# Optimization experiments

Measured on AMD Instinct MI355X. Metric: run time of the kernel, lower is better.

The kernel has to match this reference:

```python
import jax, jax.numpy as jnp
import numpy as np

B, S, D, H = 4, 2048, 1024, 16
HD = D // H


def setup_inputs() -> dict:
    key = jax.random.key(0)
    ks = jax.random.split(key, 5)
    scale = 1.0 / np.sqrt(D)
    return {
        "x": jax.random.normal(ks[0], (B, S, D), dtype=jnp.float32),
        "W_q": jax.random.normal(ks[1], (D, D), dtype=jnp.float32) * scale,
        "W_k": jax.random.normal(ks[2], (D, D), dtype=jnp.float32) * scale,
        "W_v": jax.random.normal(ks[3], (D, D), dtype=jnp.float32) * scale,
        "W_o": jax.random.normal(ks[4], (D, D), dtype=jnp.float32) * scale,
    }


def reference(x, W_q, W_k, W_v, W_o):
    # Linear with weight [out, in]: y = x @ W^T
    def proj(W):
        return jnp.einsum('bsd,ed->bshf', x, W.reshape(H, HD, D).transpose(0, 1, 2).reshape(D, D)) if False else (x @ W.T).reshape(B, S, H, HD).transpose(0, 2, 1, 3)

    q = proj(W_q)  # [B, H, S, HD]
    k = proj(W_k)
    v = proj(W_v)

    scores = jnp.einsum('bhqd,bhkd->bhqk', q, k) / jnp.sqrt(jnp.float32(HD))
    causal = jnp.triu(jnp.ones((S, S), dtype=bool), k=1)  # True above diagonal -> masked
    scores = jnp.where(causal, -jnp.inf, scores)
    probs = jax.nn.softmax(scores, axis=-1)
    out = jnp.einsum('bhqk,bhkd->bhqd', probs, v)  # [B, H, S, HD]
    out = out.transpose(0, 2, 1, 3).reshape(B, S, D)
    return out @ W_o.T
```

## Files before the change

### kernel.cpp

```cpp
#include <hip/hip_runtime.h>
#include <cstdint>
#include <cstddef>

typedef unsigned short u16;
typedef __attribute__((ext_vector_type(8))) short short8;
typedef __attribute__((ext_vector_type(4))) short short4v;
typedef __attribute__((ext_vector_type(8))) unsigned short ushort8v;
typedef __attribute__((ext_vector_type(4))) unsigned short ushort4v;
typedef __attribute__((ext_vector_type(4))) unsigned int uint4v;
typedef __attribute__((ext_vector_type(4))) float f32x4;

#define QSCALE 0.18033688011112042f
#define THR_L2 11.5417f


__device__ __forceinline__ u16 f2bf(float f) {
  unsigned int u = __builtin_bit_cast(unsigned int, f);
  u += 0x7FFFu + ((u >> 16) & 1u);
  return (u16)(u >> 16);
}

__device__ __forceinline__ void async16(const void* g, void* l) {
  __builtin_amdgcn_global_load_lds(
      (const __attribute__((address_space(1))) unsigned int*)g,
      (__attribute__((address_space(3))) unsigned int*)l, 16, 0, 0);
}

__device__ __forceinline__ float fmax3(float a, float b, float c) {
  float r;
  asm("v_max3_f32 %0, %1, %2, %3" : "=v"(r) : "v"(a), "v"(b), "v"(c));
  return r;
}

__device__ __forceinline__ unsigned int cvtpk(float lo, float hi) {
  unsigned int r;
  asm("v_cvt_pk_bf16_f32 %0, %1, %2" : "=v"(r) : "v"(lo), "v"(hi));
  return r;
}


__global__ void cvt_all(const float* __restrict__ x, const float* __restrict__ Wq,
                        const float* __restrict__ Wk, const float* __restrict__ Wv,
                        const float* __restrict__ Wo, u16* __restrict__ out) {
  const int bid = blockIdx.x;
  const float* src;
  int i;
  size_t doff;
  if (bid < 8192) {
    i = bid * 1024 + threadIdx.x * 4;
    src = x;
    doff = (size_t)i;
  } else {
    const int k = bid - 8192;
    const int wsel = k >> 10;
    i = (k & 1023) * 1024 + threadIdx.x * 4;
    src = (wsel == 0) ? Wq : (wsel == 1) ? Wk : (wsel == 2) ? Wv : Wo;
    doff = 8388608 + (size_t)wsel * 1048576 + i;
  }
  float4 v = *(const float4*)(src + i);
  ushort4v o;
  o[0] = f2bf(v.x); o[1] = f2bf(v.y); o[2] = f2bf(v.z); o[3] = f2bf(v.w);
  *(ushort4v*)(out + doff) = o;
}


template<int MODE>
__global__ __launch_bounds__(256, 3) void gemm_bt(
    const u16* __restrict__ A, const u16* __restrict__ Bw,
    void* __restrict__ Cout, int M, int N, int K)
{
  const int t = threadIdx.x;
  const int lane = t & 63, w = t >> 6;
  const int li = lane & 15, g = lane >> 4;
  const int wr = w >> 1, wc = w & 1;

  const int nx = gridDim.x;
  const int hwid = blockIdx.y * nx + blockIdx.x;
  const int cpx = (nx * gridDim.y) >> 3;
  const int lid = (hwid & 7) * cpx + (hwid >> 3);
  const int brow = (lid / nx) * 128, bcol = (lid % nx) * 128;

  __shared__ u16 As[128 * 32];
  __shared__ u16 Bs[128 * 32];

  f32x4 acc[4][4];
#pragma unroll
  for (int i = 0; i < 4; ++i)
#pragma unroll
    for (int j = 0; j < 4; ++j) acc[i][j] = f32x4{0.f, 0.f, 0.f, 0.f};

  for (int k0 = 0; k0 < K; k0 += 32) {
#pragma unroll
    for (int L = 0; L < 2; ++L) {
      const int f = t + 256 * L;
      const int row = f >> 2;
      const int cb = ((f & 3) * 16) ^ ((row & 3) << 4);
      async16(A + (size_t)(brow + row) * K + k0 + (cb >> 1),
              &As[(w * 64 + 256 * L) * 8]);
      async16(Bw + (size_t)(bcol + row) * K + k0 + (cb >> 1),
              &Bs[(w * 64 + 256 * L) * 8]);
    }
    __syncthreads();
    short8 af[4], bfr[4];
    const int ksw = (g * 8) ^ ((li & 3) << 3);
#pragma unroll
    for (int mt = 0; mt < 4; ++mt)
      af[mt] = *(const short8*)&As[(wr * 64 + mt * 16 + li) * 32 + ksw];
#pragma unroll
    for (int nt = 0; nt < 4; ++nt)
      bfr[nt] = *(const short8*)&Bs[(wc * 64 + nt * 16 + li) * 32 + ksw];
    __builtin_amdgcn_s_setprio(1);
#pragma unroll
    for (int mt = 0; mt < 4; ++mt)
#pragma unroll
      for (int nt = 0; nt < 4; ++nt)
        acc[mt][nt] = __builtin_amdgcn_mfma_f32_16x16x32_bf16(af[mt], bfr[nt], acc[mt][nt], 0, 0, 0);
    __builtin_amdgcn_s_setprio(0);
    __syncthreads();
  }

#pragma unroll
  for (int mt = 0; mt < 4; ++mt)
#pragma unroll
    for (int nt = 0; nt < 4; ++nt) {
      const int col = bcol + wc * 64 + nt * 16 + li;
#pragma unroll
      for (int r = 0; r < 4; ++r) {
        const int row = brow + wr * 64 + mt * 16 + g * 4 + r;
        float v = acc[mt][nt][r];
        if (MODE == 0) {
          const int which = col >> 10;
          const int c2 = col & 1023;
          if (which == 0) v *= QSCALE;
          const int b = row >> 11, s = row & 2047;
          const int h = c2 >> 6, hd = c2 & 63;
          ((u16*)Cout)[(size_t)which * 8388608 +
                       (((size_t)(b * 16 + h) * 2048) + s) * 64 + hd] = f2bf(v);
        } else {
          ((float*)Cout)[(size_t)row * N + col] = v;
        }
      }
    }
}


__global__ __launch_bounds__(256) void transpose_hd_s(
    const u16* __restrict__ V, u16* __restrict__ VT)
{
  const int sb = blockIdx.x;
  const int bh = blockIdx.y;
  __shared__ u16 tile[64 * 72];
  const int t = threadIdx.x;
  const int r = t >> 3;
  const int c8 = (t & 7) * 8;
  const size_t base = (size_t)bh * 2048 * 64;
#pragma unroll
  for (int half = 0; half < 2; ++half) {
    const int row = r + 32 * half;
    ushort8v v = *(const ushort8v*)(V + base + (size_t)(sb * 64 + row) * 64 + c8);
    *(ushort8v*)&tile[row * 72 + c8] = v;
  }
  __syncthreads();
#pragma unroll
  for (int half = 0; half < 2; ++half) {
    const int hd = r + 32 * half;
    ushort8v o;
#pragma unroll
    for (int j = 0; j < 8; ++j) o[j] = tile[(c8 + j) * 72 + hd];
    *(ushort8v*)(VT + base + (size_t)hd * 2048 + sb * 64 + c8) = o;
  }
}


__global__ __launch_bounds__(256, 5) void flash_attn5(
    const u16* __restrict__ Qp, const u16* __restrict__ Kp,
    const u16* __restrict__ VTp, u16* __restrict__ Oattn)
{
  const int n = blockIdx.x;
  const int xcd = n & 7, sq = n >> 3;
  const int bh = xcd * 8 + (sq >> 4);
  const int pr = sq & 15;
  const int tile0 = pr, tile1 = 31 - pr;
  const int njb0 = pr + 1;

  const int t = threadIdx.x;
  const int lane = t & 63, w = t >> 6;
  const int li = lane & 15, g = lane >> 4;

  __shared__ u16 Kl[2][4096];
  __shared__ u16 Vl[2][4096];

  const size_t bh_off = (size_t)bh * (2048 * 64);
  const int b = bh >> 4, h = bh & 15;
  const int ksw = (li & 7) << 3;

  int qbase = tile0 * 64;

  f32x4 o_acc[4];
#pragma unroll
  for (int i = 0; i < 4; ++i) o_acc[i] = f32x4{0.f, 0.f, 0.f, 0.f};
  float m_i = -1e30f, l_i = 0.f;

  auto STAGE = [&](int i, int sb) {
    const int jb = (i < njb0) ? i : (i - njb0);
#pragma unroll
    for (int L = 0; L < 2; ++L) {
      const int f = t + 256 * L;
      const int kbyte = (f * 16) ^ (((f >> 3) & 7) << 4);
      async16(Kp + bh_off + (size_t)jb * 4096 + (kbyte >> 1),
              &Kl[sb][(w * 64 + 256 * L) * 8]);
      const int vrow = f >> 3;
      const int vb = ((f & 7) * 16) ^ ((vrow & 7) << 4);
      async16(VTp + bh_off + (size_t)vrow * 2048 + jb * 64 + (vb >> 1),
              &Vl[sb][(w * 64 + 256 * L) * 8]);
    }
  };

  auto WRITEO = [&]() {
    const float inv_l = 1.f / l_i;
    const int qrow = qbase + w * 16 + li;
    u16* op = Oattn + ((size_t)(b * 2048 + qrow)) * 1024 + h * 64;
#pragma unroll
    for (int dt = 0; dt < 4; ++dt) {
      ushort4v st;
#pragma unroll
      for (int r = 0; r < 4; ++r) st[r] = f2bf(o_acc[dt][r] * inv_l);
      *(ushort4v*)(op + dt * 16 + g * 4) = st;
    }
  };

  short8 qc[2];
  {
    const u16* qp = Qp + bh_off + (size_t)(qbase + w * 16 + li) * 64 + g * 8;
    qc[0] = *(const short8*)qp;
    qc[1] = *(const short8*)(qp + 32);
  }

  STAGE(0, 0);
  asm volatile("s_waitcnt vmcnt(0)" ::: "memory");
  __builtin_amdgcn_s_barrier();

#pragma unroll 1
  for (int i = 0; i < 33; ++i) {
    const int sb = i & 1;
    if (i + 1 < 33) STAGE(i + 1, (i + 1) & 1);

    const int jb = (i < njb0) ? i : (i - njb0);
    const u16* __restrict__ Ks = &Kl[sb][0];
    const u16* __restrict__ Vs = &Vl[sb][0];

    f32x4 s_acc[4];
#pragma unroll
    for (int jt = 0; jt < 4; ++jt) s_acc[jt] = f32x4{0.f, 0.f, 0.f, 0.f};
    __builtin_amdgcn_s_setprio(1);
#pragma unroll
    for (int kc = 0; kc < 2; ++kc)
#pragma unroll
      for (int jt = 0; jt < 4; ++jt) {
        short8 kf = *(const short8*)&Ks[(jt * 16 + li) * 64 + ((kc * 32 + g * 8) ^ ksw)];
        s_acc[jt] = __builtin_amdgcn_mfma_f32_16x16x32_bf16(kf, qc[kc], s_acc[jt], 0, 0, 0);
      }
    __builtin_amdgcn_s_setprio(0);

    if (jb * 64 + 63 > qbase + w * 16) {
      const int tq = qbase + w * 16 + li - jb * 64;
#pragma unroll
      for (int jt = 0; jt < 4; ++jt)
#pragma unroll
        for (int r = 0; r < 4; ++r)
          if (jt * 16 + g * 4 + r > tq) s_acc[jt][r] = -1e30f;
    }
    float t0 = fmax3(s_acc[0][0], s_acc[0][1], s_acc[0][2]);
    float t1 = fmax3(s_acc[0][3], s_acc[1][0], s_acc[1][1]);
    float t2 = fmax3(s_acc[1][2], s_acc[1][3], s_acc[2][0]);
    float t3 = fmax3(s_acc[2][1], s_acc[2][2], s_acc[2][3]);
    float t4m = fmax3(s_acc[3][0], s_acc[3][1], s_acc[3][2]);
    float m01 = fmax3(t0, t1, s_acc[3][3]);
    float m23 = fmax3(t2, t3, t4m);
    float mm = fmaxf(m01, m23);
    mm = fmaxf(mm, __shfl_xor(mm, 16));
    mm = fmaxf(mm, __shfl_xor(mm, 32));

    if (__any((int)(mm > m_i + THR_L2))) {
      const float mn = fmaxf(m_i, mm);
      const float corr = __builtin_amdgcn_exp2f(m_i - mn);
      l_i *= corr;
#pragma unroll
      for (int dt = 0; dt < 4; ++dt) o_acc[dt] *= corr;
      m_i = mn;
    }

    float ps = 0.f;
#pragma unroll
    for (int jt = 0; jt < 4; ++jt)
#pragma unroll
      for (int r = 0; r < 4; ++r) {
        float e = __builtin_amdgcn_exp2f(s_acc[jt][r] - m_i);
        s_acc[jt][r] = e;
        ps += e;
      }
    ps += __shfl_xor(ps, 16);
    ps += __shfl_xor(ps, 32);
    l_i += ps;
    short8 pf[2];
#pragma unroll
    for (int kc = 0; kc < 2; ++kc) {
      uint4v u;
      u[0] = cvtpk(s_acc[2 * kc][0], s_acc[2 * kc][1]);
      u[1] = cvtpk(s_acc[2 * kc][2], s_acc[2 * kc][3]);
      u[2] = cvtpk(s_acc[2 * kc + 1][0], s_acc[2 * kc + 1][1]);
      u[3] = cvtpk(s_acc[2 * kc + 1][2], s_acc[2 * kc + 1][3]);
      pf[kc] = __builtin_bit_cast(short8, u);
    }

    __builtin_amdgcn_s_setprio(1);
#pragma unroll
    for (int kc = 0; kc < 2; ++kc)
#pragma unroll
      for (int dt = 0; dt < 4; ++dt) {
        const int rowb = (dt * 16 + li) * 64;
        short4v v0 = *(const short4v*)&Vs[rowb + ((kc * 32 + g * 4) ^ ksw)];
        short4v v1 = *(const short4v*)&Vs[rowb + ((kc * 32 + 16 + g * 4) ^ ksw)];
        short8 vf = __builtin_shufflevector(v0, v1, 0, 1, 2, 3, 4, 5, 6, 7);
        o_acc[dt] = __builtin_amdgcn_mfma_f32_16x16x32_bf16(vf, pf[kc], o_acc[dt], 0, 0, 0);
      }
    __builtin_amdgcn_s_setprio(0);

    asm volatile("s_waitcnt lgkmcnt(0)" ::: "memory");
    asm volatile("s_waitcnt vmcnt(0)" ::: "memory");
    __builtin_amdgcn_s_barrier();

    if (i == njb0 - 1) {
      WRITEO();
      qbase = tile1 * 64;
      const u16* qp = Qp + bh_off + (size_t)(qbase + w * 16 + li) * 64 + g * 8;
      qc[0] = *(const short8*)qp;
      qc[1] = *(const short8*)(qp + 32);
      m_i = -1e30f; l_i = 0.f;
#pragma unroll
      for (int dt = 0; dt < 4; ++dt) o_acc[dt] = f32x4{0.f, 0.f, 0.f, 0.f};
    }
  }

  WRITEO();
}


extern "C" void kernel_launch(void* const* d_in, const int* in_sizes, int n_in,
                              void* d_out, int out_size, void* d_ws, size_t ws_size,
                              hipStream_t stream) {
  const float* x  = (const float*)d_in[0];
  const float* Wq = (const float*)d_in[1];
  const float* Wk = (const float*)d_in[2];
  const float* Wv = (const float*)d_in[3];
  const float* Wo = (const float*)d_in[4];

  const size_t NX = 8388608;
  const size_t NW = 1048576;

  u16* xb  = (u16*)d_ws;
  u16* wqb = xb + NX;
  u16* wob = wqb + 3 * NW;
  u16* Qb  = wob + NW;
  u16* Kb  = Qb + NX;
  u16* Vb  = Kb + NX;
  u16* VTb = Vb + NX;
  u16* attnb = Vb;

  cvt_all<<<12288, 256, 0, stream>>>(x, Wq, Wk, Wv, Wo, xb);

  gemm_bt<0><<<dim3(24, 64), 256, 0, stream>>>(xb, wqb, Qb, 8192, 3072, 1024);

  transpose_hd_s<<<dim3(32, 64), 256, 0, stream>>>(Vb, VTb);
  flash_attn5<<<1024, 256, 0, stream>>>(Qb, Kb, VTb, attnb);

  gemm_bt<1><<<dim3(8, 64), 256, 0, stream>>>(attnb, wob, d_out, 8192, 1024, 1024);
}
```

Before: 182.7 us.

## Rewrite flash attention with 128-row query tiles and direct global K/V loads

```diff
diff --git a/kernel.cpp b/kernel.cpp
--- a/kernel.cpp
+++ b/kernel.cpp
@@ -4,10 +4,10 @@
 
 typedef unsigned short u16;
 typedef __attribute__((ext_vector_type(8))) short short8;
-typedef __attribute__((ext_vector_type(4))) short short4v;
 typedef __attribute__((ext_vector_type(8))) unsigned short ushort8v;
 typedef __attribute__((ext_vector_type(4))) unsigned short ushort4v;
 typedef __attribute__((ext_vector_type(4))) unsigned int uint4v;
+typedef __attribute__((ext_vector_type(2))) unsigned int uint2v;
 typedef __attribute__((ext_vector_type(4))) float f32x4;
 
 #define QSCALE 0.18033688011112042f
@@ -172,173 +172,180 @@
 }
 
 
-__global__ __launch_bounds__(256, 5) void flash_attn5(
+__global__ __launch_bounds__(256, 2) void flash_attn8(
     const u16* __restrict__ Qp, const u16* __restrict__ Kp,
     const u16* __restrict__ VTp, u16* __restrict__ Oattn)
 {
-  const int n = blockIdx.x;
-  const int xcd = n & 7, sq = n >> 3;
-  const int bh = xcd * 8 + (sq >> 4);
-  const int pr = sq & 15;
-  const int tile0 = pr, tile1 = 31 - pr;
-  const int njb0 = pr + 1;
+  const int id = blockIdx.x;
+  const int x8 = id & 7, r8 = id >> 3;
+  const int bh = x8 * 8 + (r8 & 7);
+  const int p  = r8 >> 3;
+  const int tile1 = 15 - p;
+  const int njb0 = 2 * p + 2;
 
   const int t = threadIdx.x;
   const int lane = t & 63, w = t >> 6;
   const int li = lane & 15, g = lane >> 4;
 
-  __shared__ u16 Kl[2][4096];
-  __shared__ u16 Vl[2][4096];
-
   const size_t bh_off = (size_t)bh * (2048 * 64);
   const int b = bh >> 4, h = bh & 15;
-  const int ksw = (li & 7) << 3;
-
-  int qbase = tile0 * 64;
-
-  f32x4 o_acc[4];
-#pragma unroll
-  for (int i = 0; i < 4; ++i) o_acc[i] = f32x4{0.f, 0.f, 0.f, 0.f};
-  float m_i = -1e30f, l_i = 0.f;
-
-  auto STAGE = [&](int i, int sb) {
+
+  int q0 = p * 128 + w * 32;
+
+  short8 qf[2][2];
+  auto LOADQ = [&]() {
+#pragma unroll
+    for (int qn = 0; qn < 2; ++qn)
+#pragma unroll
+      for (int kc = 0; kc < 2; ++kc)
+        qf[qn][kc] = *(const short8*)(Qp + bh_off +
+            (size_t)(q0 + qn * 16 + li) * 64 + kc * 32 + g * 8);
+  };
+  LOADQ();
+
+  f32x4 o_acc[4][2];
+#pragma unroll
+  for (int dt = 0; dt < 4; ++dt)
+#pragma unroll
+    for (int qn = 0; qn < 2; ++qn) o_acc[dt][qn] = f32x4{0.f, 0.f, 0.f, 0.f};
+  float m_i[2] = {-1e30f, -1e30f};
+  float l_i[2] = {0.f, 0.f};
+
+  auto WRITEO = [&]() {
+#pragma unroll
+    for (int qn = 0; qn < 2; ++qn) {
+      const float inv = 1.f / l_i[qn];
+      u16* op = Oattn + ((size_t)(b * 2048 + q0 + qn * 16 + li)) * 1024 + h * 64;
+#pragma unroll
+      for (int dt = 0; dt < 4; ++dt) {
+        ushort4v st;
+#pragma unroll
+        for (int r = 0; r < 4; ++r) st[r] = f2bf(o_acc[dt][qn][r] * inv);
+        *(ushort4v*)(op + dt * 16 + g * 4) = st;
+      }
+    }
+  };
+
+#pragma unroll 1
+  for (int i = 0; i < 34; ++i) {
     const int jb = (i < njb0) ? i : (i - njb0);
-#pragma unroll
-    for (int L = 0; L < 2; ++L) {
-      const int f = t + 256 * L;
-      const int kbyte = (f * 16) ^ (((f >> 3) & 7) << 4);
-      async16(Kp + bh_off + (size_t)jb * 4096 + (kbyte >> 1),
-              &Kl[sb][(w * 64 + 256 * L) * 8]);
-      const int vrow = f >> 3;
-      const int vb = ((f & 7) * 16) ^ ((vrow & 7) << 4);
-      async16(VTp + bh_off + (size_t)vrow * 2048 + jb * 64 + (vb >> 1),
-              &Vl[sb][(w * 64 + 256 * L) * 8]);
-    }
-  };
-
-  auto WRITEO = [&]() {
-    const float inv_l = 1.f / l_i;
-    const int qrow = qbase + w * 16 + li;
-    u16* op = Oattn + ((size_t)(b * 2048 + qrow)) * 1024 + h * 64;
-#pragma unroll
-    for (int dt = 0; dt < 4; ++dt) {
-      ushort4v st;
-#pragma unroll
-      for (int r = 0; r < 4; ++r) st[r] = f2bf(o_acc[dt][r] * inv_l);
-      *(ushort4v*)(op + dt * 16 + g * 4) = st;
-    }
-  };
-
-  short8 qc[2];
-  {
-    const u16* qp = Qp + bh_off + (size_t)(qbase + w * 16 + li) * 64 + g * 8;
-    qc[0] = *(const short8*)qp;
-    qc[1] = *(const short8*)(qp + 32);
-  }
-
-  STAGE(0, 0);
-  asm volatile("s_waitcnt vmcnt(0)" ::: "memory");
-  __builtin_amdgcn_s_barrier();
-
-#pragma unroll 1
-  for (int i = 0; i < 33; ++i) {
-    const int sb = i & 1;
-    if (i + 1 < 33) STAGE(i + 1, (i + 1) & 1);
-
-    const int jb = (i < njb0) ? i : (i - njb0);
-    const u16* __restrict__ Ks = &Kl[sb][0];
-    const u16* __restrict__ Vs = &Vl[sb][0];
-
-    f32x4 s_acc[4];
-#pragma unroll
-    for (int jt = 0; jt < 4; ++jt) s_acc[jt] = f32x4{0.f, 0.f, 0.f, 0.f};
-    __builtin_amdgcn_s_setprio(1);
-#pragma unroll
-    for (int kc = 0; kc < 2; ++kc)
-#pragma unroll
-      for (int jt = 0; jt < 4; ++jt) {
-        short8 kf = *(const short8*)&Ks[(jt * 16 + li) * 64 + ((kc * 32 + g * 8) ^ ksw)];
-        s_acc[jt] = __builtin_amdgcn_mfma_f32_16x16x32_bf16(kf, qc[kc], s_acc[jt], 0, 0, 0);
-      }
-    __builtin_amdgcn_s_setprio(0);
-
-    if (jb * 64 + 63 > qbase + w * 16) {
-      const int tq = qbase + w * 16 + li - jb * 64;
-#pragma unroll
-      for (int jt = 0; jt < 4; ++jt)
-#pragma unroll
-        for (int r = 0; r < 4; ++r)
-          if (jt * 16 + g * 4 + r > tq) s_acc[jt][r] = -1e30f;
-    }
-    float t0 = fmax3(s_acc[0][0], s_acc[0][1], s_acc[0][2]);
-    float t1 = fmax3(s_acc[0][3], s_acc[1][0], s_acc[1][1]);
-    float t2 = fmax3(s_acc[1][2], s_acc[1][3], s_acc[2][0]);
-    float t3 = fmax3(s_acc[2][1], s_acc[2][2], s_acc[2][3]);
-    float t4m = fmax3(s_acc[3][0], s_acc[3][1], s_acc[3][2]);
-    float m01 = fmax3(t0, t1, s_acc[3][3]);
-    float m23 = fmax3(t2, t3, t4m);
-    float mm = fmaxf(m01, m23);
-    mm = fmaxf(mm, __shfl_xor(mm, 16));
-    mm = fmaxf(mm, __shfl_xor(mm, 32));
-
-    if (__any((int)(mm > m_i + THR_L2))) {
-      const float mn = fmaxf(m_i, mm);
-      const float corr = __builtin_amdgcn_exp2f(m_i - mn);
-      l_i *= corr;
-#pragma unroll
-      for (int dt = 0; dt < 4; ++dt) o_acc[dt] *= corr;
-      m_i = mn;
-    }
-
-    float ps = 0.f;
-#pragma unroll
-    for (int jt = 0; jt < 4; ++jt)
-#pragma unroll
-      for (int r = 0; r < 4; ++r) {
-        float e = __builtin_amdgcn_exp2f(s_acc[jt][r] - m_i);
-        s_acc[jt][r] = e;
-        ps += e;
-      }
-    ps += __shfl_xor(ps, 16);
-    ps += __shfl_xor(ps, 32);
-    l_i += ps;
-    short8 pf[2];
-#pragma unroll
-    for (int kc = 0; kc < 2; ++kc) {
-      uint4v u;
-      u[0] = cvtpk(s_acc[2 * kc][0], s_acc[2 * kc][1]);
-      u[1] = cvtpk(s_acc[2 * kc][2], s_acc[2 * kc][3]);
-      u[2] = cvtpk(s_acc[2 * kc + 1][0], s_acc[2 * kc + 1][1]);
-      u[3] = cvtpk(s_acc[2 * kc + 1][2], s_acc[2 * kc + 1][3]);
-      pf[kc] = __builtin_bit_cast(short8, u);
-    }
-
-    __builtin_amdgcn_s_setprio(1);
-#pragma unroll
-    for (int kc = 0; kc < 2; ++kc)
-#pragma unroll
-      for (int dt = 0; dt < 4; ++dt) {
-        const int rowb = (dt * 16 + li) * 64;
-        short4v v0 = *(const short4v*)&Vs[rowb + ((kc * 32 + g * 4) ^ ksw)];
-        short4v v1 = *(const short4v*)&Vs[rowb + ((kc * 32 + 16 + g * 4) ^ ksw)];
-        short8 vf = __builtin_shufflevector(v0, v1, 0, 1, 2, 3, 4, 5, 6, 7);
-        o_acc[dt] = __builtin_amdgcn_mfma_f32_16x16x32_bf16(vf, pf[kc], o_acc[dt], 0, 0, 0);
-      }
-    __builtin_amdgcn_s_setprio(0);
-
-    asm volatile("s_waitcnt lgkmcnt(0)" ::: "memory");
-    asm volatile("s_waitcnt vmcnt(0)" ::: "memory");
-    __builtin_amdgcn_s_barrier();
+    const bool active = (jb * 64 <= q0 + 31);
+    if (active) {
+      short8 kf[2][4];
+#pragma unroll
+      for (int kc = 0; kc < 2; ++kc)
+#pragma unroll
+        for (int jt = 0; jt < 4; ++jt)
+          kf[kc][jt] = *(const short8*)(Kp + bh_off +
+              (size_t)(jb * 64 + jt * 16 + li) * 64 + kc * 32 + g * 8);
+
+      f32x4 s[2][4];
+#pragma unroll
+      for (int qn = 0; qn < 2; ++qn)
+#pragma unroll
+        for (int jt = 0; jt < 4; ++jt) s[qn][jt] = f32x4{0.f, 0.f, 0.f, 0.f};
+      __builtin_amdgcn_s_setprio(1);
+#pragma unroll
+      for (int kc = 0; kc < 2; ++kc)
+#pragma unroll
+        for (int jt = 0; jt < 4; ++jt) {
+          s[0][jt] = __builtin_amdgcn_mfma_f32_16x16x32_bf16(kf[kc][jt], qf[0][kc], s[0][jt], 0, 0, 0);
+          s[1][jt] = __builtin_amdgcn_mfma_f32_16x16x32_bf16(kf[kc][jt], qf[1][kc], s[1][jt], 0, 0, 0);
+        }
+      __builtin_amdgcn_s_setprio(0);
+
+      float mx[2];
+      bool need = false;
+#pragma unroll
+      for (int qn = 0; qn < 2; ++qn) {
+        if (jb * 64 + 63 > q0 + qn * 16) {
+          const int tq = q0 + qn * 16 + li - jb * 64;
+#pragma unroll
+          for (int jt = 0; jt < 4; ++jt)
+#pragma unroll
+            for (int r = 0; r < 4; ++r)
+              if (jt * 16 + g * 4 + r > tq) s[qn][jt][r] = -1e30f;
+        }
+        float t0 = fmax3(s[qn][0][0], s[qn][0][1], s[qn][0][2]);
+        float t1 = fmax3(s[qn][0][3], s[qn][1][0], s[qn][1][1]);
+        float t2 = fmax3(s[qn][1][2], s[qn][1][3], s[qn][2][0]);
+        float t3 = fmax3(s[qn][2][1], s[qn][2][2], s[qn][2][3]);
+        float t4m = fmax3(s[qn][3][0], s[qn][3][1], s[qn][3][2]);
+        float m01 = fmax3(t0, t1, s[qn][3][3]);
+        float m23 = fmax3(t2, t3, t4m);
+        float mm = fmaxf(m01, m23);
+        mm = fmaxf(mm, __shfl_xor(mm, 16));
+        mm = fmaxf(mm, __shfl_xor(mm, 32));
+        mx[qn] = mm;
+        need = need || (mm > m_i[qn] + THR_L2);
+      }
+
+      if (__any((int)need)) {
+#pragma unroll
+        for (int qn = 0; qn < 2; ++qn) {
+          const float mn = fmaxf(m_i[qn], mx[qn]);
+          const float corr = __builtin_amdgcn_exp2f(m_i[qn] - mn);
+          l_i[qn] *= corr;
+#pragma unroll
+          for (int dt = 0; dt < 4; ++dt) o_acc[dt][qn] *= corr;
+          m_i[qn] = mn;
+        }
+      }
+
+      short8 pf[2][2];
+#pragma unroll
+      for (int qn = 0; qn < 2; ++qn) {
+        const float mi = m_i[qn];
+        float ps = 0.f;
+#pragma unroll
+        for (int jt = 0; jt < 4; ++jt)
+#pragma unroll
+          for (int r = 0; r < 4; ++r) {
+            float e = __builtin_amdgcn_exp2f(s[qn][jt][r] - mi);
+            s[qn][jt][r] = e;
+            ps += e;
+          }
+        ps += __shfl_xor(ps, 16);
+        ps += __shfl_xor(ps, 32);
+        l_i[qn] += ps;
+#pragma unroll
+        for (int kc = 0; kc < 2; ++kc) {
+          uint4v u;
+          u[0] = cvtpk(s[qn][2 * kc][0], s[qn][2 * kc][1]);
+          u[1] = cvtpk(s[qn][2 * kc][2], s[qn][2 * kc][3]);
+          u[2] = cvtpk(s[qn][2 * kc + 1][0], s[qn][2 * kc + 1][1]);
+          u[3] = cvtpk(s[qn][2 * kc + 1][2], s[qn][2 * kc + 1][3]);
+          pf[qn][kc] = __builtin_bit_cast(short8, u);
+        }
+      }
+
+      __builtin_amdgcn_s_setprio(1);
+#pragma unroll
+      for (int kc = 0; kc < 2; ++kc)
+#pragma unroll
+        for (int dt = 0; dt < 4; ++dt) {
+          const u16* vp = VTp + bh_off + (size_t)(dt * 16 + li) * 2048 +
+                          jb * 64 + kc * 32 + g * 4;
+          uint2v lo = *(const uint2v*)vp;
+          uint2v hi8 = *(const uint2v*)(vp + 16);
+          uint4v u4; u4[0] = lo[0]; u4[1] = lo[1]; u4[2] = hi8[0]; u4[3] = hi8[1];
+          short8 vf = __builtin_bit_cast(short8, u4);
+          o_acc[dt][0] = __builtin_amdgcn_mfma_f32_16x16x32_bf16(vf, pf[0][kc], o_acc[dt][0], 0, 0, 0);
+          o_acc[dt][1] = __builtin_amdgcn_mfma_f32_16x16x32_bf16(vf, pf[1][kc], o_acc[dt][1], 0, 0, 0);
+        }
+      __builtin_amdgcn_s_setprio(0);
+    }
 
     if (i == njb0 - 1) {
       WRITEO();
-      qbase = tile1 * 64;
-      const u16* qp = Qp + bh_off + (size_t)(qbase + w * 16 + li) * 64 + g * 8;
-      qc[0] = *(const short8*)qp;
-      qc[1] = *(const short8*)(qp + 32);
-      m_i = -1e30f; l_i = 0.f;
-#pragma unroll
-      for (int dt = 0; dt < 4; ++dt) o_acc[dt] = f32x4{0.f, 0.f, 0.f, 0.f};
+      q0 = tile1 * 128 + w * 32;
+      LOADQ();
+#pragma unroll
+      for (int qn = 0; qn < 2; ++qn) {
+        m_i[qn] = -1e30f; l_i[qn] = 0.f;
+#pragma unroll
+        for (int dt = 0; dt < 4; ++dt) o_acc[dt][qn] = f32x4{0.f, 0.f, 0.f, 0.f};
+      }
     }
   }
 
@@ -372,7 +379,7 @@
   gemm_bt<0><<<dim3(24, 64), 256, 0, stream>>>(xb, wqb, Qb, 8192, 3072, 1024);
 
   transpose_hd_s<<<dim3(32, 64), 256, 0, stream>>>(Vb, VTb);
-  flash_attn5<<<1024, 256, 0, stream>>>(Qb, Kb, VTb, attnb);
+  flash_attn8<<<512, 256, 0, stream>>>(Qb, Kb, VTb, attnb);
 
   gemm_bt<1><<<dim3(8, 64), 256, 0, stream>>>(attnb, wob, d_out, 8192, 1024, 1024);
 }
```

After: 290.7 us. 1.59x slower.
